# Performance work log

Hardware: AMD Instinct MI355X
Metric: run time of the kernel (lower is better)

## Reference

```python
import jax, jax.numpy as jnp
import numpy as np

PATCH = 16  # insize // num

def setup_inputs() -> dict:
    key = jax.random.key(0)
    k1, k2, k3 = jax.random.split(key, 3)
    B, C, H, W = 16, 2048, 64, 64
    P, Cr = 16, 128  # num*num patches, c // reduction
    x = jax.random.normal(k1, (B, C, H, W), dtype=jnp.float32)
    # stacked per-patch SE weights (Linear bias=False): fc1 [Cr, C], fc2 [C, Cr]
    W1 = jax.random.normal(k2, (P, Cr, C), dtype=jnp.float32) * (1.0 / np.sqrt(C))
    W2 = jax.random.normal(k3, (P, C, Cr), dtype=jnp.float32) * (1.0 / np.sqrt(Cr))
    return {"x": x, "W1": W1, "W2": W2}

def reference(x, W1, W2):
    # Faithful to original: every one of the P SE blocks pools the SAME
    # fixed patch x[..., ps:2ps, ps:2ps] (the loop indices are unused).
    ps = PATCH
    patch = x[..., ps:2 * ps, ps:2 * ps]          # [B, C, ps, ps]
    y = jnp.mean(patch, axis=(-2, -1))            # global avg pool -> [B, C]
    h = jax.nn.relu(jnp.einsum('pkc,bc->pbk', W1, y))   # [P, B, C/r]
    att = jax.nn.sigmoid(jnp.einsum('pck,pbk->pbc', W2, h))  # [P, B, C]
    return att[..., None, None]                   # [P, B, C, 1, 1] (stacked list)
```

## Files before the change

kernel.cpp:

```cpp
#include <hip/hip_runtime.h>
#include <math.h>

#define B_  16
#define C_  2048
#define H_  64
#define W_  64
#define P_  16
#define CR_ 128
#define PS_ 16

__global__ void k_mean(const float* __restrict__ x, float* __restrict__ y) {
    int wave = blockIdx.x * (blockDim.x >> 6) + (threadIdx.x >> 6);
    int lane = threadIdx.x & 63;
    const float* base = x + (size_t)wave * (H_ * W_) + PS_ * W_ + PS_;
    int row = lane >> 2;
    int col = (lane & 3) * 4;
    float4 v = *reinterpret_cast<const float4*>(base + row * W_ + col);
    float s = v.x + v.y + v.z + v.w;
    #pragma unroll
    for (int m = 32; m >= 1; m >>= 1) s += __shfl_xor(s, m, 64);
    if (lane == 0) y[wave] = s * (1.0f / 256.0f);
}

__global__ void k_fc1(const float* __restrict__ w1, const float* __restrict__ y,
                      float* __restrict__ h) {
    int wid  = blockIdx.x * (blockDim.x >> 6) + (threadIdx.x >> 6);
    int lane = threadIdx.x & 63;
    int p = wid >> 7, k = wid & 127;

    const float4* wr = reinterpret_cast<const float4*>(w1) + (size_t)wid * (C_ / 4);
    const float4* yv = reinterpret_cast<const float4*>(y);

    float acc[B_];
    #pragma unroll
    for (int b = 0; b < B_; ++b) acc[b] = 0.0f;

    #pragma unroll
    for (int i = 0; i < C_ / 256; ++i) {
        int c4 = i * 64 + lane;
        float4 w4 = wr[c4];
        #pragma unroll
        for (int b = 0; b < B_; ++b) {
            float4 v = yv[b * (C_ / 4) + c4];
            acc[b] += w4.x * v.x;
            acc[b] += w4.y * v.y;
            acc[b] += w4.z * v.z;
            acc[b] += w4.w * v.w;
        }
    }

    #pragma unroll
    for (int b = 0; b < B_; ++b) {
        #pragma unroll
        for (int m = 32; m >= 1; m >>= 1) acc[b] += __shfl_xor(acc[b], m, 64);
    }

    float v = acc[0];
    #pragma unroll
    for (int b = 1; b < B_; ++b) v = (lane == b) ? acc[b] : v;

    if (lane < B_) h[(p * B_ + lane) * CR_ + k] = fmaxf(v, 0.0f);
}

__global__ void __launch_bounds__(256) k_fc2(const float* __restrict__ w2,
                                             const float* __restrict__ h,
                                             float* __restrict__ out) {
    __shared__ float hs[B_ * CR_];

    int wib  = threadIdx.x >> 6;
    int wid  = blockIdx.x * 4 + wib;
    int lane = threadIdx.x & 63;
    int p  = wid >> 7;
    int c0 = (wid & 127) << 4;
    int row = lane >> 2;
    int q   = lane & 3;

    const float4* hsrc = reinterpret_cast<const float4*>(h + (size_t)p * B_ * CR_);
    float4* hdst = reinterpret_cast<float4*>(hs);
    #pragma unroll
    for (int i = 0; i < 2; ++i)
        hdst[threadIdx.x + i * 256] = hsrc[threadIdx.x + i * 256];
    __syncthreads();

    const float4* wr = reinterpret_cast<const float4*>(w2)
                     + ((size_t)p * C_ + c0 + row) * (CR_ / 4);
    const float4* hv = reinterpret_cast<const float4*>(hs);

    float acc[B_];
    #pragma unroll
    for (int b = 0; b < B_; ++b) acc[b] = 0.0f;

    #pragma unroll
    for (int j = 0; j < 8; ++j) {
        float4 w4 = wr[q + 4 * j];
        #pragma unroll
        for (int b = 0; b < B_; ++b) {
            float4 h4 = hv[b * (CR_ / 4) + q + 4 * j];
            acc[b] += w4.x * h4.x;
            acc[b] += w4.y * h4.y;
            acc[b] += w4.z * h4.z;
            acc[b] += w4.w * h4.w;
        }
    }

    #pragma unroll
    for (int b = 0; b < B_; ++b) {
        acc[b] += __shfl_xor(acc[b], 1, 64);
        acc[b] += __shfl_xor(acc[b], 2, 64);
    }

    #pragma unroll
    for (int i = 0; i < 4; ++i) {
        float v = acc[i];
        v = (q == 1) ? acc[4 + i]  : v;
        v = (q == 2) ? acc[8 + i]  : v;
        v = (q == 3) ? acc[12 + i] : v;
        int b = q * 4 + i;
        out[(((size_t)p * B_ + b) << 11) + c0 + row] = 1.0f / (1.0f + expf(-v));
    }
}

extern "C" void kernel_launch(void* const* d_in, const int* in_sizes, int n_in,
                              void* d_out, int out_size, void* d_ws, size_t ws_size,
                              hipStream_t stream) {
    const float* x  = (const float*)d_in[0];
    const float* w1 = (const float*)d_in[1];
    const float* w2 = (const float*)d_in[2];
    float* out = (float*)d_out;
    float* y = (float*)d_ws;
    float* h = y + B_ * C_;

    k_mean<<<(B_ * C_) / 4, 256, 0, stream>>>(x, y);
    k_fc1<<<(P_ * CR_) / 4, 256, 0, stream>>>(w1, y, h);
    k_fc2<<<(P_ * C_ / 16) / 4, 256, 0, stream>>>(w2, h, out);
}
```

Baseline: 48.02 us.

## Stage pooled vector in LDS for fc1, two rows per wave, four channels per wave in mean

The mean kernel now has each wave reduce four channels, with four independent loads and shuffle chains, and uses a quarter of the blocks. fc1 copies the full 128 KB pooled vector y into shared memory once per block. Each wave then computes two weight rows with register prefetch of the next weight chunk, instead of re-reading y from global memory for every row. The fc2 inner update is rewritten as a single combined dot-product expression. The 128 KB shared allocation limits occupancy to about one block per CU, and each of the 256 blocks pays for a full copy of y.

New measurement: 39.00 us. -18.8%, faster.

```diff
diff --git a/kernel.cpp b/kernel.cpp
--- a/kernel.cpp
+++ b/kernel.cpp
@@ -12,54 +12,90 @@
 __global__ void k_mean(const float* __restrict__ x, float* __restrict__ y) {
     int wave = blockIdx.x * (blockDim.x >> 6) + (threadIdx.x >> 6);
     int lane = threadIdx.x & 63;
-    const float* base = x + (size_t)wave * (H_ * W_) + PS_ * W_ + PS_;
     int row = lane >> 2;
     int col = (lane & 3) * 4;
-    float4 v = *reinterpret_cast<const float4*>(base + row * W_ + col);
-    float s = v.x + v.y + v.z + v.w;
+    const float* base = x + (size_t)wave * 4 * (H_ * W_) + PS_ * W_ + PS_
+                      + row * W_ + col;
+    float4 v0 = *reinterpret_cast<const float4*>(base);
+    float4 v1 = *reinterpret_cast<const float4*>(base + H_ * W_);
+    float4 v2 = *reinterpret_cast<const float4*>(base + 2 * H_ * W_);
+    float4 v3 = *reinterpret_cast<const float4*>(base + 3 * H_ * W_);
+    float s0 = v0.x + v0.y + v0.z + v0.w;
+    float s1 = v1.x + v1.y + v1.z + v1.w;
+    float s2 = v2.x + v2.y + v2.z + v2.w;
+    float s3 = v3.x + v3.y + v3.z + v3.w;
     #pragma unroll
-    for (int m = 32; m >= 1; m >>= 1) s += __shfl_xor(s, m, 64);
-    if (lane == 0) y[wave] = s * (1.0f / 256.0f);
+    for (int m = 32; m >= 1; m >>= 1) {
+        s0 += __shfl_xor(s0, m, 64);
+        s1 += __shfl_xor(s1, m, 64);
+        s2 += __shfl_xor(s2, m, 64);
+        s3 += __shfl_xor(s3, m, 64);
+    }
+    float v = s0;
+    v = (lane == 1) ? s1 : v;
+    v = (lane == 2) ? s2 : v;
+    v = (lane == 3) ? s3 : v;
+    if (lane < 4) y[wave * 4 + lane] = v * (1.0f / 256.0f);
 }
 
-__global__ void k_fc1(const float* __restrict__ w1, const float* __restrict__ y,
-                      float* __restrict__ h) {
-    int wid  = blockIdx.x * (blockDim.x >> 6) + (threadIdx.x >> 6);
-    int lane = threadIdx.x & 63;
-    int p = wid >> 7, k = wid & 127;
+__global__ void __launch_bounds__(256) k_fc1(const float* __restrict__ w1,
+                                             const float* __restrict__ y,
+                                             float* __restrict__ h) {
+    __shared__ float ys[B_ * C_];
+    int tid  = threadIdx.x;
+    int wib  = tid >> 6;
+    int lane = tid & 63;
 
-    const float4* wr = reinterpret_cast<const float4*>(w1) + (size_t)wid * (C_ / 4);
-    const float4* yv = reinterpret_cast<const float4*>(y);
+    const float4* ysrc = reinterpret_cast<const float4*>(y);
+    float4* ydst = reinterpret_cast<float4*>(ys);
+    #pragma unroll 8
+    for (int i = 0; i < 32; ++i)
+        ydst[tid + 256 * i] = ysrc[tid + 256 * i];
+    __syncthreads();
 
-    float acc[B_];
+    int r0 = blockIdx.x * 8 + wib * 2;
+    const float4* wr0 = reinterpret_cast<const float4*>(w1) + (size_t)r0 * (C_ / 4);
+    const float4* wr1 = wr0 + (C_ / 4);
+
+    float acc0[B_], acc1[B_];
     #pragma unroll
-    for (int b = 0; b < B_; ++b) acc[b] = 0.0f;
+    for (int b = 0; b < B_; ++b) { acc0[b] = 0.0f; acc1[b] = 0.0f; }
 
+    float4 pa = wr0[lane];
+    float4 pb = wr1[lane];
     #pragma unroll
-    for (int i = 0; i < C_ / 256; ++i) {
-        int c4 = i * 64 + lane;
-        float4 w4 = wr[c4];
+    for (int i = 0; i < 8; ++i) {
+        float4 wa = pa, wb = pb;
+        if (i < 7) { pa = wr0[(i + 1) * 64 + lane]; pb = wr1[(i + 1) * 64 + lane]; }
+        const float4* yrow = reinterpret_cast<const float4*>(ys) + i * 64 + lane;
         #pragma unroll
         for (int b = 0; b < B_; ++b) {
-            float4 v = yv[b * (C_ / 4) + c4];
-            acc[b] += w4.x * v.x;
-            acc[b] += w4.y * v.y;
-            acc[b] += w4.z * v.z;
-            acc[b] += w4.w * v.w;
+            float4 v = yrow[b * (C_ / 4)];
+            acc0[b] += wa.x * v.x + wa.y * v.y + wa.z * v.z + wa.w * v.w;
+            acc1[b] += wb.x * v.x + wb.y * v.y + wb.z * v.z + wb.w * v.w;
         }
     }
 
     #pragma unroll
     for (int b = 0; b < B_; ++b) {
         #pragma unroll
-        for (int m = 32; m >= 1; m >>= 1) acc[b] += __shfl_xor(acc[b], m, 64);
+        for (int m = 32; m >= 1; m >>= 1) {
+            acc0[b] += __shfl_xor(acc0[b], m, 64);
+            acc1[b] += __shfl_xor(acc1[b], m, 64);
+        }
     }
 
-    float v = acc[0];
+    float v0 = acc0[0], v1 = acc1[0];
     #pragma unroll
-    for (int b = 1; b < B_; ++b) v = (lane == b) ? acc[b] : v;
-
-    if (lane < B_) h[(p * B_ + lane) * CR_ + k] = fmaxf(v, 0.0f);
+    for (int b = 1; b < B_; ++b) {
+        v0 = (lane == b) ? acc0[b] : v0;
+        v1 = (lane == b) ? acc1[b] : v1;
+    }
+    if (lane < B_) {
+        int p = r0 >> 7, k = r0 & 127;
+        h[(p * B_ + lane) * CR_ + k]     = fmaxf(v0, 0.0f);
+        h[(p * B_ + lane) * CR_ + k + 1] = fmaxf(v1, 0.0f);
+    }
 }
 
 __global__ void __launch_bounds__(256) k_fc2(const float* __restrict__ w2,
@@ -96,10 +132,7 @@
         #pragma unroll
         for (int b = 0; b < B_; ++b) {
             float4 h4 = hv[b * (CR_ / 4) + q + 4 * j];
-            acc[b] += w4.x * h4.x;
-            acc[b] += w4.y * h4.y;
-            acc[b] += w4.z * h4.z;
-            acc[b] += w4.w * h4.w;
+            acc[b] += w4.x * h4.x + w4.y * h4.y + w4.z * h4.z + w4.w * h4.w;
         }
     }
 
@@ -130,7 +163,7 @@
     float* y = (float*)d_ws;
     float* h = y + B_ * C_;
 
-    k_mean<<<(B_ * C_) / 4, 256, 0, stream>>>(x, y);
-    k_fc1<<<(P_ * CR_) / 4, 256, 0, stream>>>(w1, y, h);
+    k_mean<<<(B_ * C_ / 4) / 4, 256, 0, stream>>>(x, y);
+    k_fc1<<<256, 256, 0, stream>>>(w1, y, h);
     k_fc2<<<(P_ * C_ / 16) / 4, 256, 0, stream>>>(w2, h, out);
 }
```
